# Kernel tuning notes

Hardware: AMD Instinct MI355X
Metric: run time of the kernel (lower is better)

## Reference

```python
import jax, jax.numpy as jnp
import numpy as np

N_ROWS = 200000
N_REFS = 2000000
X_DIM = 128
UNITS = 128


def setup_inputs() -> dict:
    key = jax.random.key(0)
    ks = jax.random.split(key, 8)
    X = jax.random.normal(ks[0], (N_ROWS, X_DIM), dtype=jnp.float32)
    ref_a = jax.random.randint(ks[1], (N_REFS,), 0, N_ROWS, dtype=jnp.int32)
    ref_b = jax.random.randint(ks[2], (N_REFS,), 0, N_ROWS, dtype=jnp.int32)
    backref = jax.random.randint(ks[3], (N_REFS,), 0, N_ROWS, dtype=jnp.int32)
    # Glorot-uniform-ish init for the three projections
    limit = np.sqrt(6.0 / (X_DIM + UNITS)).astype(np.float32)
    W_local = jax.random.uniform(ks[4], (X_DIM, UNITS), jnp.float32, -limit, limit)
    W_filter = jax.random.uniform(ks[5], (X_DIM, UNITS), jnp.float32, -limit, limit)
    W_neighbor = jax.random.uniform(ks[6], (X_DIM, UNITS), jnp.float32, -limit, limit)
    b = jnp.zeros((UNITS,), jnp.float32)
    b_neighbor = jnp.zeros((UNITS,), jnp.float32)
    return dict(X=X, ref_a=ref_a, ref_b=ref_b, backref=backref,
                W_local=W_local, W_filter=W_filter, W_neighbor=W_neighbor,
                b=b, b_neighbor=b_neighbor)


def reference(X, ref_a, ref_b, backref, W_local, W_filter, W_neighbor, b, b_neighbor):
    # Dense projections [N, units]
    XW_local = X @ W_local
    XW_filter = X @ W_filter
    XW_neighbor = X @ W_neighbor
    # wl2_convolution: gather pairs, combine (add + bias + inner relu), scatter-sum via backref
    msg = jax.nn.relu(XW_neighbor[ref_a] + XW_neighbor[ref_b] + b_neighbor)  # [M, units]
    X_conv = jax.ops.segment_sum(msg, backref, num_segments=X.shape[0])      # [N, units]
    X_agg = XW_local + XW_filter * X_conv + b
    return jax.nn.relu(X_agg)
```

## Files before the change

kernel.cpp:

```cpp
#include <hip/hip_runtime.h>


constexpr int DIM = 128;
constexpr int CAP = 40;

typedef _Float16 half_t;
typedef __attribute__((ext_vector_type(8))) _Float16 half8;
typedef __attribute__((ext_vector_type(4))) float f32x4;

__global__ __launch_bounds__(256) void transpose_w_k(
    const float* __restrict__ Wl, const float* __restrict__ Wf,
    const float* __restrict__ Wn, half_t* __restrict__ WlT,
    half_t* __restrict__ WfT, half_t* __restrict__ WnT) {
  __shared__ float t0[32][33], t1[32][33], t2[32][33];
  const int bx = (blockIdx.x & 3) * 32;
  const int by = (blockIdx.x >> 2) * 32;
  const int x = threadIdx.x & 31;
  const int y4 = (threadIdx.x >> 5) * 4;
#pragma unroll
  for (int i = 0; i < 4; ++i) {
    t0[y4 + i][x] = Wl[(by + y4 + i) * DIM + bx + x];
    t1[y4 + i][x] = Wf[(by + y4 + i) * DIM + bx + x];
    t2[y4 + i][x] = Wn[(by + y4 + i) * DIM + bx + x];
  }
  __syncthreads();
#pragma unroll
  for (int i = 0; i < 4; ++i) {
    WlT[(bx + y4 + i) * DIM + by + x] = (half_t)t0[x][y4 + i];
    WfT[(bx + y4 + i) * DIM + by + x] = (half_t)t1[x][y4 + i];
    WnT[(bx + y4 + i) * DIM + by + x] = (half_t)t2[x][y4 + i];
  }
}

__global__ __launch_bounds__(256) void fuseA_k(
    const float* __restrict__ X, const half_t* __restrict__ WnT,
    const float* __restrict__ bn, half_t* __restrict__ XWnh,
    const int* __restrict__ ra, const int* __restrict__ rb,
    const int* __restrict__ br, int* __restrict__ cnt,
    int2* __restrict__ slots, int Nrows, int E, int nbBlocks) {
  __shared__ half_t WT[DIM][136];
  const int g = blockIdx.x >> 1;
  const int tid = threadIdx.x;

  if (blockIdx.x & 1) {
    const int stride = nbBlocks * 256;
    for (int e = g * 256 + tid; e < E; e += stride) {
      const int row = br[e];
      const int pos = atomicAdd(&cnt[row], 1);
      if (pos < CAP) slots[(long)pos * Nrows + row] = make_int2(ra[e], rb[e]);
    }
    return;
  }

  for (int id = tid; id < 2048; id += 256) {
    const int u = id >> 4, c = (id & 15) * 8;
    *(half8*)(&WT[u][c]) = *(const half8*)(WnT + u * DIM + c);
  }
  __syncthreads();
  const int wave = tid >> 6, lane = tid & 63;
  const int ln = lane & 15, quad = lane >> 4;
  const long r0 = (long)g * 128 + wave * 32;
  f32x4 acc[2][8];
#pragma unroll
  for (int mt = 0; mt < 2; ++mt)
#pragma unroll
    for (int n = 0; n < 8; ++n) acc[mt][n] = (f32x4){0.f, 0.f, 0.f, 0.f};

  for (int kt = 0; kt < DIM; kt += 32) {
    half8 afr[2];
#pragma unroll
    for (int mt = 0; mt < 2; ++mt) {
      long row = r0 + mt * 16 + ln;
      if (row >= Nrows) row = Nrows - 1;
      const float* xp = X + row * DIM + kt + quad * 8;
      const float4 x0 = *(const float4*)xp;
      const float4 x1 = *(const float4*)(xp + 4);
      half8 a;
      a[0] = (half_t)x0.x; a[1] = (half_t)x0.y; a[2] = (half_t)x0.z; a[3] = (half_t)x0.w;
      a[4] = (half_t)x1.x; a[5] = (half_t)x1.y; a[6] = (half_t)x1.z; a[7] = (half_t)x1.w;
      afr[mt] = a;
    }
#pragma unroll
    for (int n = 0; n < 8; ++n) {
      const half8 b = *(const half8*)(&WT[n * 16 + ln][kt + quad * 8]);
      acc[0][n] = __builtin_amdgcn_mfma_f32_16x16x32_f16(afr[0], b, acc[0][n], 0, 0, 0);
      acc[1][n] = __builtin_amdgcn_mfma_f32_16x16x32_f16(afr[1], b, acc[1][n], 0, 0, 0);
    }
  }
#pragma unroll
  for (int n = 0; n < 8; ++n) {
    const int col = n * 16 + ln;
    const float bv = 0.5f * bn[col];
#pragma unroll
    for (int mt = 0; mt < 2; ++mt)
#pragma unroll
      for (int r = 0; r < 4; ++r) {
        const long row = r0 + mt * 16 + quad * 4 + r;
        if (row < Nrows) XWnh[row * DIM + col] = (half_t)(acc[mt][n][r] + bv);
      }
  }
}

__global__ __launch_bounds__(256) void gather_k(
    const half_t* __restrict__ XWnh, const int* __restrict__ cnt,
    const int2* __restrict__ slots, half_t* __restrict__ convh, int Nrows) {
  const int wave = threadIdx.x >> 6;
  const long row = (long)blockIdx.x * 4 + wave;
  if (row >= Nrows) return;
  const int lane = threadIdx.x & 63;
  const int sub = lane >> 4;
  const int sl = lane & 15;
  int c = cnt[row];
  if (c > CAP) c = CAP;
  float acc[8] = {0.f, 0.f, 0.f, 0.f, 0.f, 0.f, 0.f, 0.f};
  for (int p = sub; p < c; p += 4) {
    const int2 ab = slots[(long)p * Nrows + row];
    const half8 ha = *(const half8*)(XWnh + (long)ab.x * DIM + sl * 8);
    const half8 hb = *(const half8*)(XWnh + (long)ab.y * DIM + sl * 8);
#pragma unroll
    for (int j = 0; j < 8; ++j)
      acc[j] += fmaxf((float)ha[j] + (float)hb[j], 0.f);
  }
#pragma unroll
  for (int j = 0; j < 8; ++j) {
    acc[j] += __shfl_xor(acc[j], 16);
    acc[j] += __shfl_xor(acc[j], 32);
  }
  if (sub == 0) {
    half8 o;
#pragma unroll
    for (int j = 0; j < 8; ++j) o[j] = (half_t)acc[j];
    *(half8*)(convh + row * DIM + sl * 8) = o;
  }
}

__global__ __launch_bounds__(256, 2) void final_mfma_k(
    const float* __restrict__ X, const half_t* __restrict__ WlT,
    const half_t* __restrict__ WfT, const float* __restrict__ bias,
    const half_t* __restrict__ convh, float* __restrict__ out, int Nrows) {
  __shared__ half_t WTl[DIM][136];
  __shared__ half_t WTf[DIM][136];
  const int tid = threadIdx.x;
  for (int id = tid; id < 2048; id += 256) {
    const int u = id >> 4, c = (id & 15) * 8;
    *(half8*)(&WTl[u][c]) = *(const half8*)(WlT + u * DIM + c);
    *(half8*)(&WTf[u][c]) = *(const half8*)(WfT + u * DIM + c);
  }
  __syncthreads();
  const int wave = tid >> 6, lane = tid & 63;
  const int ln = lane & 15, quad = lane >> 4;
  const long r0 = (long)blockIdx.x * 128 + wave * 32;
  f32x4 accl[2][8], accf[2][8];
#pragma unroll
  for (int mt = 0; mt < 2; ++mt)
#pragma unroll
    for (int n = 0; n < 8; ++n) {
      accl[mt][n] = (f32x4){0.f, 0.f, 0.f, 0.f};
      accf[mt][n] = (f32x4){0.f, 0.f, 0.f, 0.f};
    }

  for (int kt = 0; kt < DIM; kt += 32) {
    half8 afr[2];
#pragma unroll
    for (int mt = 0; mt < 2; ++mt) {
      long row = r0 + mt * 16 + ln;
      if (row >= Nrows) row = Nrows - 1;
      const float* xp = X + row * DIM + kt + quad * 8;
      const float4 x0 = *(const float4*)xp;
      const float4 x1 = *(const float4*)(xp + 4);
      half8 a;
      a[0] = (half_t)x0.x; a[1] = (half_t)x0.y; a[2] = (half_t)x0.z; a[3] = (half_t)x0.w;
      a[4] = (half_t)x1.x; a[5] = (half_t)x1.y; a[6] = (half_t)x1.z; a[7] = (half_t)x1.w;
      afr[mt] = a;
    }
#pragma unroll
    for (int n = 0; n < 8; ++n) {
      const half8 bl = *(const half8*)(&WTl[n * 16 + ln][kt + quad * 8]);
      const half8 bf = *(const half8*)(&WTf[n * 16 + ln][kt + quad * 8]);
      accl[0][n] = __builtin_amdgcn_mfma_f32_16x16x32_f16(afr[0], bl, accl[0][n], 0, 0, 0);
      accl[1][n] = __builtin_amdgcn_mfma_f32_16x16x32_f16(afr[1], bl, accl[1][n], 0, 0, 0);
      accf[0][n] = __builtin_amdgcn_mfma_f32_16x16x32_f16(afr[0], bf, accf[0][n], 0, 0, 0);
      accf[1][n] = __builtin_amdgcn_mfma_f32_16x16x32_f16(afr[1], bf, accf[1][n], 0, 0, 0);
    }
  }
#pragma unroll
  for (int n = 0; n < 8; ++n) {
    const int col = n * 16 + ln;
    const float bv = bias[col];
#pragma unroll
    for (int mt = 0; mt < 2; ++mt)
#pragma unroll
      for (int r = 0; r < 4; ++r) {
        const long row = r0 + mt * 16 + quad * 4 + r;
        if (row < Nrows) {
          const float cv = (float)convh[row * DIM + col];
          out[row * DIM + col] = fmaxf(accl[mt][n][r] + accf[mt][n][r] * cv + bv, 0.f);
        }
      }
  }
}

extern "C" void kernel_launch(void* const* d_in, const int* in_sizes, int n_in,
                              void* d_out, int out_size, void* d_ws, size_t ws_size,
                              hipStream_t stream) {
  const float* X  = (const float*)d_in[0];
  const int* ra   = (const int*)d_in[1];
  const int* rb   = (const int*)d_in[2];
  const int* br   = (const int*)d_in[3];
  const float* Wl = (const float*)d_in[4];
  const float* Wf = (const float*)d_in[5];
  const float* Wn = (const float*)d_in[6];
  const float* b  = (const float*)d_in[7];
  const float* bn = (const float*)d_in[8];
  float* out = (float*)d_out;

  const int N = in_sizes[0] / DIM;
  const int E = in_sizes[1];

  half_t* XWnh = (half_t*)d_ws;
  half_t* convh = XWnh + (size_t)N * DIM;
  half_t* WlT = convh + (size_t)N * DIM;
  half_t* WfT = WlT + DIM * DIM;
  half_t* WnT = WfT + DIM * DIM;
  int* cnt = (int*)(WnT + DIM * DIM);
  int2* slots = (int2*)(cnt + ((N + 1) & ~1));

  hipMemsetAsync(cnt, 0, (size_t)N * sizeof(int), stream);
  transpose_w_k<<<16, 256, 0, stream>>>(Wl, Wf, Wn, WlT, WfT, WnT);

  const int nbBlocks = (N + 127) / 128;
  fuseA_k<<<2 * nbBlocks, 256, 0, stream>>>(X, WnT, bn, XWnh, ra, rb, br, cnt,
                                            slots, N, E, nbBlocks);
  gather_k<<<(N + 3) / 4, 256, 0, stream>>>(XWnh, cnt, slots, convh, N);
  final_mfma_k<<<nbBlocks, 256, 0, stream>>>(X, WlT, WfT, b, convh, out, N);
}
```

Measured before the change: 540.3 us.

## Fuse gather into final MFMA kernel with software-pipelined neighbor loads

Merges the separate gather kernel into the final projection kernel. Each block gathers and relu-sums messages for its 128 rows into shared memory, so the conv intermediate no longer round-trips through global memory and one launch goes away. The gather processes two rows per wave with a 4-deep register prefetch pipeline, and it adds the two halves in fp16 before the relu. The final stage reuses a single shared weight buffer for the local and filter projections in turn and keeps the X fragments in registers. The fused kernel has much less parallelism for the latency-bound gather (4 waves per 128 rows instead of one wave per row), which risks exposing memory latency, and the fp16 add adds a small precision change.

Measured after the change: 630.8 us. 16.7% more time.

```diff
diff --git a/kernel.cpp b/kernel.cpp
--- a/kernel.cpp
+++ b/kernel.cpp
@@ -7,6 +7,13 @@
 typedef _Float16 half_t;
 typedef __attribute__((ext_vector_type(8))) _Float16 half8;
 typedef __attribute__((ext_vector_type(4))) float f32x4;
+
+__device__ inline half8 h8z() {
+  half8 z;
+#pragma unroll
+  for (int q = 0; q < 8; ++q) z[q] = (half_t)0.f;
+  return z;
+}
 
 __global__ __launch_bounds__(256) void transpose_w_k(
     const float* __restrict__ Wl, const float* __restrict__ Wf,
@@ -101,88 +108,138 @@
   }
 }
 
-__global__ __launch_bounds__(256) void gather_k(
-    const half_t* __restrict__ XWnh, const int* __restrict__ cnt,
-    const int2* __restrict__ slots, half_t* __restrict__ convh, int Nrows) {
-  const int wave = threadIdx.x >> 6;
-  const long row = (long)blockIdx.x * 4 + wave;
-  if (row >= Nrows) return;
-  const int lane = threadIdx.x & 63;
-  const int sub = lane >> 4;
-  const int sl = lane & 15;
-  int c = cnt[row];
-  if (c > CAP) c = CAP;
-  float acc[8] = {0.f, 0.f, 0.f, 0.f, 0.f, 0.f, 0.f, 0.f};
-  for (int p = sub; p < c; p += 4) {
-    const int2 ab = slots[(long)p * Nrows + row];
-    const half8 ha = *(const half8*)(XWnh + (long)ab.x * DIM + sl * 8);
-    const half8 hb = *(const half8*)(XWnh + (long)ab.y * DIM + sl * 8);
-#pragma unroll
-    for (int j = 0; j < 8; ++j)
-      acc[j] += fmaxf((float)ha[j] + (float)hb[j], 0.f);
-  }
-#pragma unroll
-  for (int j = 0; j < 8; ++j) {
-    acc[j] += __shfl_xor(acc[j], 16);
-    acc[j] += __shfl_xor(acc[j], 32);
-  }
-  if (sub == 0) {
-    half8 o;
-#pragma unroll
-    for (int j = 0; j < 8; ++j) o[j] = (half_t)acc[j];
-    *(half8*)(convh + row * DIM + sl * 8) = o;
-  }
-}
-
-__global__ __launch_bounds__(256, 2) void final_mfma_k(
+__global__ __launch_bounds__(256, 2) void gatherfinal_k(
     const float* __restrict__ X, const half_t* __restrict__ WlT,
     const half_t* __restrict__ WfT, const float* __restrict__ bias,
-    const half_t* __restrict__ convh, float* __restrict__ out, int Nrows) {
-  __shared__ half_t WTl[DIM][136];
-  __shared__ half_t WTf[DIM][136];
+    const half_t* __restrict__ XWnh, const int* __restrict__ cnt,
+    const int2* __restrict__ slots, float* __restrict__ out, int Nrows) {
+  __shared__ half_t conv[128][136];
+  __shared__ half_t WT[128][136];
   const int tid = threadIdx.x;
-  for (int id = tid; id < 2048; id += 256) {
-    const int u = id >> 4, c = (id & 15) * 8;
-    *(half8*)(&WTl[u][c]) = *(const half8*)(WlT + u * DIM + c);
-    *(half8*)(&WTf[u][c]) = *(const half8*)(WfT + u * DIM + c);
-  }
-  __syncthreads();
   const int wave = tid >> 6, lane = tid & 63;
+  const long rbase = (long)blockIdx.x * 128 + wave * 32;
+
+  {
+    const int hw  = lane >> 5;
+    const int sub = (lane >> 4) & 1;
+    const int sl  = lane & 15;
+    int cw = 0;
+    {
+      const long rr = rbase + lane;
+      if (lane < 32 && rr < Nrows) {
+        const int c = cnt[rr];
+        cw = c > CAP ? CAP : c;
+      }
+    }
+    for (int i = 0; i < 32; i += 2) {
+      const long row = rbase + i + hw;
+      const int c0 = __shfl(cw, i), c1 = __shfl(cw, i + 1);
+      const int myc = hw ? c1 : c0;
+      const int cmax = c0 > c1 ? c0 : c1;
+      const int nit = (cmax + 1) >> 1;
+      const long rowc = row < Nrows ? row : 0;
+      float acc[8] = {0.f, 0.f, 0.f, 0.f, 0.f, 0.f, 0.f, 0.f};
+      half8 A0 = h8z(), B0 = h8z(), A1 = h8z(), B1 = h8z();
+      half8 A2 = h8z(), B2 = h8z(), A3 = h8z(), B3 = h8z();
+#define GF_ISSUE(J, A, B)                                              \
+  {                                                                    \
+    const int p_ = sub + 2 * (J);                                      \
+    if (p_ < myc) {                                                    \
+      const int2 ab_ = slots[(long)p_ * Nrows + rowc];                 \
+      A = *(const half8*)(XWnh + (long)ab_.x * DIM + sl * 8);          \
+      B = *(const half8*)(XWnh + (long)ab_.y * DIM + sl * 8);          \
+    }                                                                  \
+  }
+#define GF_CONSUME(J, A, B)                                            \
+  {                                                                    \
+    if (sub + 2 * (J) < myc) {                                         \
+      const half8 s_ = A + B;                        \
+      _Pragma("unroll") for (int q_ = 0; q_ < 8; ++q_)                 \
+          acc[q_] += fmaxf((float)s_[q_], 0.f);                        \
+    }                                                                  \
+  }
+      GF_ISSUE(0, A0, B0);
+      GF_ISSUE(1, A1, B1);
+      GF_ISSUE(2, A2, B2);
+      GF_ISSUE(3, A3, B3);
+      for (int j = 0; j < nit; ++j) {
+        GF_CONSUME(j, A0, B0);
+        A0 = A1; B0 = B1; A1 = A2; B1 = B2; A2 = A3; B2 = B3;
+        GF_ISSUE(j + 4, A3, B3);
+      }
+#undef GF_ISSUE
+#undef GF_CONSUME
+#pragma unroll
+      for (int q = 0; q < 8; ++q) acc[q] += __shfl_xor(acc[q], 16);
+      if (row < Nrows && sub == 0) {
+        half8 o;
+#pragma unroll
+        for (int q = 0; q < 8; ++q) o[q] = (half_t)acc[q];
+        *(half8*)(&conv[wave * 32 + i + hw][sl * 8]) = o;
+      }
+    }
+  }
+
   const int ln = lane & 15, quad = lane >> 4;
-  const long r0 = (long)blockIdx.x * 128 + wave * 32;
-  f32x4 accl[2][8], accf[2][8];
-#pragma unroll
-  for (int mt = 0; mt < 2; ++mt)
-#pragma unroll
-    for (int n = 0; n < 8; ++n) {
-      accl[mt][n] = (f32x4){0.f, 0.f, 0.f, 0.f};
-      accf[mt][n] = (f32x4){0.f, 0.f, 0.f, 0.f};
-    }
-
-  for (int kt = 0; kt < DIM; kt += 32) {
-    half8 afr[2];
-#pragma unroll
-    for (int mt = 0; mt < 2; ++mt) {
-      long row = r0 + mt * 16 + ln;
-      if (row >= Nrows) row = Nrows - 1;
-      const float* xp = X + row * DIM + kt + quad * 8;
-      const float4 x0 = *(const float4*)xp;
-      const float4 x1 = *(const float4*)(xp + 4);
+
+  half8 afr[2][4];
+#pragma unroll
+  for (int mt = 0; mt < 2; ++mt) {
+    long arow = rbase + mt * 16 + ln;
+    if (arow >= Nrows) arow = Nrows - 1;
+    const float* xbase = X + arow * DIM;
+#pragma unroll
+    for (int kt = 0; kt < 4; ++kt) {
+      const float4 x0 = *(const float4*)(xbase + kt * 32 + quad * 8);
+      const float4 x1 = *(const float4*)(xbase + kt * 32 + quad * 8 + 4);
       half8 a;
       a[0] = (half_t)x0.x; a[1] = (half_t)x0.y; a[2] = (half_t)x0.z; a[3] = (half_t)x0.w;
       a[4] = (half_t)x1.x; a[5] = (half_t)x1.y; a[6] = (half_t)x1.z; a[7] = (half_t)x1.w;
-      afr[mt] = a;
-    }
+      afr[mt][kt] = a;
+    }
+  }
+
+  for (int id = tid; id < 2048; id += 256) {
+    const int u = id >> 4, c = (id & 15) * 8;
+    *(half8*)(&WT[u][c]) = *(const half8*)(WlT + u * DIM + c);
+  }
+  __syncthreads();
+
+  f32x4 accl[2][8];
+#pragma unroll
+  for (int mt = 0; mt < 2; ++mt)
+#pragma unroll
+    for (int n = 0; n < 8; ++n) accl[mt][n] = (f32x4){0.f, 0.f, 0.f, 0.f};
+#pragma unroll
+  for (int kt = 0; kt < 4; ++kt)
 #pragma unroll
     for (int n = 0; n < 8; ++n) {
-      const half8 bl = *(const half8*)(&WTl[n * 16 + ln][kt + quad * 8]);
-      const half8 bf = *(const half8*)(&WTf[n * 16 + ln][kt + quad * 8]);
-      accl[0][n] = __builtin_amdgcn_mfma_f32_16x16x32_f16(afr[0], bl, accl[0][n], 0, 0, 0);
-      accl[1][n] = __builtin_amdgcn_mfma_f32_16x16x32_f16(afr[1], bl, accl[1][n], 0, 0, 0);
-      accf[0][n] = __builtin_amdgcn_mfma_f32_16x16x32_f16(afr[0], bf, accf[0][n], 0, 0, 0);
-      accf[1][n] = __builtin_amdgcn_mfma_f32_16x16x32_f16(afr[1], bf, accf[1][n], 0, 0, 0);
-    }
-  }
+      const half8 bb = *(const half8*)(&WT[n * 16 + ln][kt * 32 + quad * 8]);
+      accl[0][n] = __builtin_amdgcn_mfma_f32_16x16x32_f16(afr[0][kt], bb, accl[0][n], 0, 0, 0);
+      accl[1][n] = __builtin_amdgcn_mfma_f32_16x16x32_f16(afr[1][kt], bb, accl[1][n], 0, 0, 0);
+    }
+  __syncthreads();
+
+  for (int id = tid; id < 2048; id += 256) {
+    const int u = id >> 4, c = (id & 15) * 8;
+    *(half8*)(&WT[u][c]) = *(const half8*)(WfT + u * DIM + c);
+  }
+  __syncthreads();
+
+  f32x4 accf[2][8];
+#pragma unroll
+  for (int mt = 0; mt < 2; ++mt)
+#pragma unroll
+    for (int n = 0; n < 8; ++n) accf[mt][n] = (f32x4){0.f, 0.f, 0.f, 0.f};
+#pragma unroll
+  for (int kt = 0; kt < 4; ++kt)
+#pragma unroll
+    for (int n = 0; n < 8; ++n) {
+      const half8 bb = *(const half8*)(&WT[n * 16 + ln][kt * 32 + quad * 8]);
+      accf[0][n] = __builtin_amdgcn_mfma_f32_16x16x32_f16(afr[0][kt], bb, accf[0][n], 0, 0, 0);
+      accf[1][n] = __builtin_amdgcn_mfma_f32_16x16x32_f16(afr[1][kt], bb, accf[1][n], 0, 0, 0);
+    }
+
 #pragma unroll
   for (int n = 0; n < 8; ++n) {
     const int col = n * 16 + ln;
@@ -191,10 +248,10 @@
     for (int mt = 0; mt < 2; ++mt)
 #pragma unroll
       for (int r = 0; r < 4; ++r) {
-        const long row = r0 + mt * 16 + quad * 4 + r;
-        if (row < Nrows) {
-          const float cv = (float)convh[row * DIM + col];
-          out[row * DIM + col] = fmaxf(accl[mt][n][r] + accf[mt][n][r] * cv + bv, 0.f);
+        const long orow = rbase + mt * 16 + quad * 4 + r;
+        if (orow < Nrows) {
+          const float cv = (float)conv[wave * 32 + mt * 16 + quad * 4 + r][col];
+          out[orow * DIM + col] = fmaxf(accl[mt][n][r] + accf[mt][n][r] * cv + bv, 0.f);
         }
       }
   }
@@ -218,8 +275,7 @@
   const int E = in_sizes[1];
 
   half_t* XWnh = (half_t*)d_ws;
-  half_t* convh = XWnh + (size_t)N * DIM;
-  half_t* WlT = convh + (size_t)N * DIM;
+  half_t* WlT = XWnh + (size_t)N * DIM;
   half_t* WfT = WlT + DIM * DIM;
   half_t* WnT = WfT + DIM * DIM;
   int* cnt = (int*)(WnT + DIM * DIM);
@@ -231,6 +287,6 @@
   const int nbBlocks = (N + 127) / 128;
   fuseA_k<<<2 * nbBlocks, 256, 0, stream>>>(X, WnT, bn, XWnh, ra, rb, br, cnt,
                                             slots, N, E, nbBlocks);
-  gather_k<<<(N + 3) / 4, 256, 0, stream>>>(XWnh, cnt, slots, convh, N);
-  final_mfma_k<<<nbBlocks, 256, 0, stream>>>(X, WlT, WfT, b, convh, out, N);
-}
+  gatherfinal_k<<<nbBlocks, 256, 0, stream>>>(X, WlT, WfT, b, XWnh, cnt,
+                                              slots, out, N);
+}
```

## Split final GEMM into two column halves to raise occupancy

Applied to the files above, without the earlier changes.

The final fused kernel now loads only half of each transposed weight matrix into shared memory at a time and processes output columns in two passes, halving LDS and accumulator registers so four blocks per CU can be resident instead of two. The X fragments are loaded once up front for all K steps and reused across both halves. This adds an extra barrier and weight reload per block and keeps more A-fragment registers live.

After: 512.7 us. 5.1% less time.

```diff
diff --git a/kernel.cpp b/kernel.cpp
--- a/kernel.cpp
+++ b/kernel.cpp
@@ -134,69 +134,80 @@
   }
 }
 
-__global__ __launch_bounds__(256, 2) void final_mfma_k(
+__global__ __launch_bounds__(256, 4) void final_mfma_k(
     const float* __restrict__ X, const half_t* __restrict__ WlT,
     const half_t* __restrict__ WfT, const float* __restrict__ bias,
     const half_t* __restrict__ convh, float* __restrict__ out, int Nrows) {
-  __shared__ half_t WTl[DIM][136];
-  __shared__ half_t WTf[DIM][136];
+  __shared__ half_t WTl[64][136];
+  __shared__ half_t WTf[64][136];
   const int tid = threadIdx.x;
-  for (int id = tid; id < 2048; id += 256) {
-    const int u = id >> 4, c = (id & 15) * 8;
-    *(half8*)(&WTl[u][c]) = *(const half8*)(WlT + u * DIM + c);
-    *(half8*)(&WTf[u][c]) = *(const half8*)(WfT + u * DIM + c);
-  }
-  __syncthreads();
   const int wave = tid >> 6, lane = tid & 63;
   const int ln = lane & 15, quad = lane >> 4;
   const long r0 = (long)blockIdx.x * 128 + wave * 32;
-  f32x4 accl[2][8], accf[2][8];
-#pragma unroll
-  for (int mt = 0; mt < 2; ++mt)
-#pragma unroll
-    for (int n = 0; n < 8; ++n) {
-      accl[mt][n] = (f32x4){0.f, 0.f, 0.f, 0.f};
-      accf[mt][n] = (f32x4){0.f, 0.f, 0.f, 0.f};
-    }
-
-  for (int kt = 0; kt < DIM; kt += 32) {
-    half8 afr[2];
-#pragma unroll
-    for (int mt = 0; mt < 2; ++mt) {
-      long row = r0 + mt * 16 + ln;
-      if (row >= Nrows) row = Nrows - 1;
-      const float* xp = X + row * DIM + kt + quad * 8;
-      const float4 x0 = *(const float4*)xp;
-      const float4 x1 = *(const float4*)(xp + 4);
+
+  half8 afr[2][4];
+#pragma unroll
+  for (int mt = 0; mt < 2; ++mt) {
+    long row = r0 + mt * 16 + ln;
+    if (row >= Nrows) row = Nrows - 1;
+    const float* xbase = X + row * DIM;
+#pragma unroll
+    for (int kt = 0; kt < 4; ++kt) {
+      const float4 x0 = *(const float4*)(xbase + kt * 32 + quad * 8);
+      const float4 x1 = *(const float4*)(xbase + kt * 32 + quad * 8 + 4);
       half8 a;
       a[0] = (half_t)x0.x; a[1] = (half_t)x0.y; a[2] = (half_t)x0.z; a[3] = (half_t)x0.w;
       a[4] = (half_t)x1.x; a[5] = (half_t)x1.y; a[6] = (half_t)x1.z; a[7] = (half_t)x1.w;
-      afr[mt] = a;
-    }
-#pragma unroll
-    for (int n = 0; n < 8; ++n) {
-      const half8 bl = *(const half8*)(&WTl[n * 16 + ln][kt + quad * 8]);
-      const half8 bf = *(const half8*)(&WTf[n * 16 + ln][kt + quad * 8]);
-      accl[0][n] = __builtin_amdgcn_mfma_f32_16x16x32_f16(afr[0], bl, accl[0][n], 0, 0, 0);
-      accl[1][n] = __builtin_amdgcn_mfma_f32_16x16x32_f16(afr[1], bl, accl[1][n], 0, 0, 0);
-      accf[0][n] = __builtin_amdgcn_mfma_f32_16x16x32_f16(afr[0], bf, accf[0][n], 0, 0, 0);
-      accf[1][n] = __builtin_amdgcn_mfma_f32_16x16x32_f16(afr[1], bf, accf[1][n], 0, 0, 0);
-    }
-  }
-#pragma unroll
-  for (int n = 0; n < 8; ++n) {
-    const int col = n * 16 + ln;
-    const float bv = bias[col];
+      afr[mt][kt] = a;
+    }
+  }
+
+  for (int hf = 0; hf < 2; ++hf) {
+    if (hf) __syncthreads();
+    for (int id = tid; id < 1024; id += 256) {
+      const int u = id >> 4, c = (id & 15) * 8;
+      const size_t src = (size_t)(hf * 64 + u) * DIM + c;
+      *(half8*)(&WTl[u][c]) = *(const half8*)(WlT + src);
+      *(half8*)(&WTf[u][c]) = *(const half8*)(WfT + src);
+    }
+    __syncthreads();
+
+    f32x4 accl[2][4], accf[2][4];
 #pragma unroll
     for (int mt = 0; mt < 2; ++mt)
 #pragma unroll
-      for (int r = 0; r < 4; ++r) {
-        const long row = r0 + mt * 16 + quad * 4 + r;
-        if (row < Nrows) {
-          const float cv = (float)convh[row * DIM + col];
-          out[row * DIM + col] = fmaxf(accl[mt][n][r] + accf[mt][n][r] * cv + bv, 0.f);
+      for (int n = 0; n < 4; ++n) {
+        accl[mt][n] = (f32x4){0.f, 0.f, 0.f, 0.f};
+        accf[mt][n] = (f32x4){0.f, 0.f, 0.f, 0.f};
+      }
+#pragma unroll
+    for (int kt = 0; kt < 4; ++kt)
+#pragma unroll
+      for (int n = 0; n < 4; ++n) {
+        const half8 bl = *(const half8*)(&WTl[n * 16 + ln][kt * 32 + quad * 8]);
+        const half8 bf = *(const half8*)(&WTf[n * 16 + ln][kt * 32 + quad * 8]);
+        accl[0][n] = __builtin_amdgcn_mfma_f32_16x16x32_f16(afr[0][kt], bl, accl[0][n], 0, 0, 0);
+        accl[1][n] = __builtin_amdgcn_mfma_f32_16x16x32_f16(afr[1][kt], bl, accl[1][n], 0, 0, 0);
+        accf[0][n] = __builtin_amdgcn_mfma_f32_16x16x32_f16(afr[0][kt], bf, accf[0][n], 0, 0, 0);
+        accf[1][n] = __builtin_amdgcn_mfma_f32_16x16x32_f16(afr[1][kt], bf, accf[1][n], 0, 0, 0);
+      }
+
+#pragma unroll
+    for (int n = 0; n < 4; ++n) {
+      const int col = hf * 64 + n * 16 + ln;
+      const float bv = bias[col];
+#pragma unroll
+      for (int mt = 0; mt < 2; ++mt)
+#pragma unroll
+        for (int r = 0; r < 4; ++r) {
+          const long orow = r0 + mt * 16 + quad * 4 + r;
+          if (orow < Nrows) {
+            const float cv = (float)convh[orow * DIM + col];
+            out[orow * DIM + col] =
+                fmaxf(accl[mt][n][r] + accf[mt][n][r] * cv + bv, 0.f);
+          }
         }
-      }
+    }
   }
 }
 
```
